# Kernel tuning notes

Measured on AMD Instinct MI355X. Metric: run time of the kernel, lower is better.

The kernel has to match this reference:

```python
import jax, jax.numpy as jnp
import numpy as np

M, K = 16384, 1024
E, N = 8, 5632  # N = 2 * intermediate (gate+up packed); intermediate = 2816
TOPK = 2


def setup_inputs() -> dict:
    key = jax.random.key(0)
    ks = jax.random.split(key, 5)
    return {
        "hidden_states": jax.random.normal(ks[0], (M, K), jnp.float32) * 0.05,
        "w1": jax.random.normal(ks[1], (E, N, K), jnp.float32) * 0.02,
        "w2": jax.random.normal(ks[2], (E, K, N // 2), jnp.float32) * 0.02,
        "topk_weights": jax.random.uniform(ks[3], (M, TOPK), jnp.float32),
        "topk_ids": jax.random.randint(ks[4], (M, TOPK), 0, E, jnp.int32),
    }


def reference(hidden_states, w1, w2, topk_weights, topk_ids):
    # hidden_states: [M, K]; w1: [E, N, K]; w2: [E, K, N//2]
    # topk_weights / topk_ids: [M, TOPK]
    m, k = hidden_states.shape
    e_num, n, _ = w1.shape
    topk = topk_ids.shape[1]
    half = n // 2
    out = jnp.zeros((m, topk, k), dtype=hidden_states.dtype)
    # Loop over the small fixed set of experts; each iteration is a dense GEMM
    # masked by the routing assignment (faithful to the grouped-GEMM math).
    for e in range(e_num):
        h1 = jnp.einsum('mk,nk->mn', hidden_states, w1[e])          # [M, N]
        gate, up = h1[:, :half], h1[:, half:]
        h2 = jax.nn.silu(gate) * up                                  # silu_and_mul
        o = jnp.einsum('mh,kh->mk', h2, w2[e])                       # [M, K]
        mask = (topk_ids == e).astype(o.dtype)                       # [M, TOPK]
        out = out + mask[:, :, None] * o[:, None, :]
    # multiply routed weights and sum over top-k slots
    return jnp.einsum('mtk,mt->mk', out, topk_weights)
```

## Files before the change

kernel.cpp:

```cpp
#include <hip/hip_runtime.h>
#include <hip/hip_bf16.h>

#define M_TOK 16384
#define K_DIM 1024
#define E_NUM 8
#define N_DIM 5632
#define HALF_N 2816
#define TOPK 2
#define NPAIR (M_TOK * TOPK)
#define BM 128
#define BK 64
#define BH1 128
#define BN2 256
#define NDESC (NPAIR / BM + E_NUM)
#define NHB1 (HALF_N / BH1)
#define NNB2 (K_DIM / BN2)

typedef short s16x4 __attribute__((ext_vector_type(4)));
typedef short s16x8 __attribute__((ext_vector_type(8)));
typedef float f32x4 __attribute__((ext_vector_type(4)));

__device__ __forceinline__ short f2bf(float f) {
  union { __hip_bfloat16 h; short s; } c;
  c.h = __float2bfloat16(f);
  return c.s;
}

__device__ __forceinline__ float bf2f(unsigned short s) {
  union { float f; unsigned u; } c;
  c.u = ((unsigned)s) << 16;
  return c.f;
}

__device__ __forceinline__ void gload_lds16(const void* g, void* l) {
  __builtin_amdgcn_global_load_lds(
      (const __attribute__((address_space(1))) unsigned int*)g,
      (__attribute__((address_space(3))) unsigned int*)l, 16, 0, 0);
}

__device__ __forceinline__ int xcd_work(int bid, int nwg) {
  const int xcd = bid & 7, loc = bid >> 3;
  const int q = nwg >> 3, r = nwg & 7;
  return (xcd < r ? xcd * (q + 1) : r * (q + 1) + (xcd - r) * q) + loc;
}

__global__ void cvt_f32_bf16_k(const float4* __restrict__ src,
                               s16x4* __restrict__ dst, int n4) {
  int i = blockIdx.x * blockDim.x + threadIdx.x;
  int stride = gridDim.x * blockDim.x;
  for (; i < n4; i += stride) {
    float4 f = src[i];
    s16x4 o = { f2bf(f.x), f2bf(f.y), f2bf(f.z), f2bf(f.w) };
    dst[i] = o;
  }
}

__global__ void moe_count(const int* __restrict__ ids, int* __restrict__ cnt) {
  const int p = blockIdx.x * 256 + threadIdx.x;
  const int e = ids[p];
  const int lane = threadIdx.x & 63;
  __shared__ int h[E_NUM];
  if (threadIdx.x < E_NUM) h[threadIdx.x] = 0;
  __syncthreads();
#pragma unroll
  for (int ex = 0; ex < E_NUM; ++ex) {
    unsigned long long m = __ballot(e == ex);
    if (lane == 0 && m) atomicAdd(&h[ex], __popcll(m));
  }
  __syncthreads();
  if (threadIdx.x < E_NUM) atomicAdd(&cnt[threadIdx.x], h[threadIdx.x]);
}

__global__ void moe_build(const int* __restrict__ cnt, int* __restrict__ offs,
                          int4* __restrict__ desc) {
  if (blockIdx.x == 0 && threadIdx.x == 0) {
    int o = 0, d = 0;
    for (int e = 0; e < E_NUM; ++e) {
      offs[e] = o;
      int end = o + cnt[e];
      for (int s = o; s < end; s += BM) desc[d++] = make_int4(e, s, end, 0);
      o = end;
    }
    offs[E_NUM] = o;
    while (d < NDESC) desc[d++] = make_int4(-1, 0, 0, 0);
  }
}

__global__ void moe_scatter(const int* __restrict__ ids, const float* __restrict__ tw,
                            const int* __restrict__ offs, int* __restrict__ fill,
                            int* __restrict__ tok, float* __restrict__ wgt,
                            int* __restrict__ inv) {
  const int p = blockIdx.x * 256 + threadIdx.x;
  const int e = ids[p];
  const int lane = threadIdx.x & 63;
  const int w = threadIdx.x >> 6;
  __shared__ int wcnt[4][E_NUM];
  __shared__ int wpre[4][E_NUM];
  __shared__ int base[E_NUM];
  const unsigned long long lt = (1ull << lane) - 1ull;
  int myrank = 0;
#pragma unroll
  for (int ex = 0; ex < E_NUM; ++ex) {
    unsigned long long m = __ballot(e == ex);
    if (e == ex) myrank = (int)__popcll(m & lt);
    if (lane == 0) wcnt[w][ex] = (int)__popcll(m);
  }
  __syncthreads();
  if (threadIdx.x < E_NUM) {
    const int ex = threadIdx.x;
    int s = 0;
#pragma unroll
    for (int ww = 0; ww < 4; ++ww) { wpre[ww][ex] = s; s += wcnt[ww][ex]; }
    base[ex] = atomicAdd(&fill[ex], s);
  }
  __syncthreads();
  const int pos = offs[e] + base[e] + wpre[w][e] + myrank;
  tok[pos] = p >> 1;
  wgt[pos] = tw[p];
  inv[p] = pos;
}

__global__ void moe_gather(const float* __restrict__ hs, const int* __restrict__ tok,
                           unsigned short* __restrict__ hsb) {
  const int pos = blockIdx.x;
  const int m = tok[pos];
  const int t = threadIdx.x;
  const float4* s = (const float4*)(hs + (size_t)m * K_DIM) + t * 2;
  const float4 a = s[0], b = s[1];
  s16x8 o = { f2bf(a.x), f2bf(a.y), f2bf(a.z), f2bf(a.w),
              f2bf(b.x), f2bf(b.y), f2bf(b.z), f2bf(b.w) };
  *(s16x8*)(hsb + (size_t)pos * K_DIM + t * 8) = o;
}

__launch_bounds__(512)
__global__ void moe_gemm1(const unsigned short* __restrict__ hsb,
                          const unsigned short* __restrict__ w1b,
                          const int4* __restrict__ desc,
                          unsigned short* __restrict__ h2) {
  const int work = xcd_work(blockIdx.x, NHB1 * NDESC);
  const int di = work / NHB1;
  const int hb = work - di * NHB1;
  const int4 d = desc[di];
  const int e = d.x;
  if (e < 0) return;
  const int pos0 = d.y, eend = d.z;
  const int h0 = hb * BH1;

  __shared__ __align__(16) unsigned short As[BM * BK];
  __shared__ __align__(16) unsigned short Gs[BH1 * BK];
  __shared__ __align__(16) unsigned short Us[BH1 * BK];

  const int tid = threadIdx.x;
  const int lane = tid & 63;
  const int wid = tid >> 6;
  const int wr = wid >> 2;
  const int wc = wid & 3;

  const unsigned short* Ab = hsb + (size_t)pos0 * K_DIM;
  const unsigned short* Gb = w1b + ((size_t)e * N_DIM + h0) * K_DIM;
  const unsigned short* Ub = Gb + (size_t)HALF_N * K_DIM;

  f32x4 accg[4][2], accu[4][2];
  const f32x4 z = {0.f, 0.f, 0.f, 0.f};
#pragma unroll
  for (int i = 0; i < 4; ++i)
#pragma unroll
    for (int j = 0; j < 2; ++j) { accg[i][j] = z; accu[i][j] = z; }

  const int lrow = lane >> 3;
  const int scol = ((lane & 7) ^ lrow) << 3;
  const int fr = lane & 15;
  const int fq = lane >> 4;
  const int sw = fr & 7;

  for (int kt = 0; kt < K_DIM / BK; ++kt) {
    const int k0 = kt * BK;
#pragma unroll
    for (int c = 0; c < 2; ++c) {
      const int seg = c * 8 + wid;
      const int row = seg * 8 + lrow;
      gload_lds16(Ab + (size_t)row * K_DIM + k0 + scol, &As[seg * 512]);
      gload_lds16(Gb + (size_t)row * K_DIM + k0 + scol, &Gs[seg * 512]);
      gload_lds16(Ub + (size_t)row * K_DIM + k0 + scol, &Us[seg * 512]);
    }
    __syncthreads();
#pragma unroll
    for (int s = 0; s < 2; ++s) {
      const int coff = (((s * 4 + fq) ^ sw) << 3);
      s16x8 af[4];
#pragma unroll
      for (int i = 0; i < 4; ++i)
        af[i] = *(const s16x8*)&As[(64 * wr + 16 * i + fr) * BK + coff];
      s16x8 gf[2], uf[2];
#pragma unroll
      for (int j = 0; j < 2; ++j) {
        const int hr = (32 * wc + 16 * j + fr) * BK + coff;
        gf[j] = *(const s16x8*)&Gs[hr];
        uf[j] = *(const s16x8*)&Us[hr];
      }
#pragma unroll
      for (int i = 0; i < 4; ++i)
#pragma unroll
        for (int j = 0; j < 2; ++j) {
          accg[i][j] = __builtin_amdgcn_mfma_f32_16x16x32_bf16(af[i], gf[j], accg[i][j], 0, 0, 0);
          accu[i][j] = __builtin_amdgcn_mfma_f32_16x16x32_bf16(af[i], uf[j], accu[i][j], 0, 0, 0);
        }
    }
    __syncthreads();
  }

  const int vlim = eend - pos0;
#pragma unroll
  for (int i = 0; i < 4; ++i) {
#pragma unroll
    for (int rr = 0; rr < 4; ++rr) {
      const int row = 64 * wr + 16 * i + fq * 4 + rr;
      if (row < vlim) {
        unsigned short* dst = h2 + (size_t)(pos0 + row) * HALF_N + h0 + 32 * wc;
#pragma unroll
        for (int j = 0; j < 2; ++j) {
          const float g = accg[i][j][rr];
          const float u = accu[i][j][rr];
          const float sg = g / (1.0f + __expf(-g));
          dst[16 * j + fr] = (unsigned short)f2bf(sg * u);
        }
      }
    }
  }
}

__launch_bounds__(512)
__global__ void moe_gemm2(const unsigned short* __restrict__ h2,
                          const unsigned short* __restrict__ w2b,
                          const int4* __restrict__ desc,
                          const float* __restrict__ wgt,
                          unsigned short* __restrict__ opair) {
  const int work = xcd_work(blockIdx.x, NNB2 * NDESC);
  const int di = work >> 2;
  const int nb = work & 3;
  const int4 d = desc[di];
  const int e = d.x;
  if (e < 0) return;
  const int pos0 = d.y, eend = d.z;
  const int n0 = nb * BN2;

  __shared__ __align__(16) unsigned short As[BM * BK];
  __shared__ __align__(16) unsigned short Bs[BN2 * BK];

  const int tid = threadIdx.x;
  const int lane = tid & 63;
  const int wid = tid >> 6;
  const int wr = wid >> 2;
  const int wc = wid & 3;

  const unsigned short* Ab = h2 + (size_t)pos0 * HALF_N;
  const unsigned short* Bb = w2b + ((size_t)e * K_DIM + n0) * HALF_N;

  f32x4 acc[4][4];
  const f32x4 z = {0.f, 0.f, 0.f, 0.f};
#pragma unroll
  for (int i = 0; i < 4; ++i)
#pragma unroll
    for (int j = 0; j < 4; ++j) acc[i][j] = z;

  const int lrow = lane >> 3;
  const int scol = ((lane & 7) ^ lrow) << 3;
  const int fr = lane & 15;
  const int fq = lane >> 4;
  const int sw = fr & 7;

  for (int ht = 0; ht < HALF_N / BK; ++ht) {
    const int k0 = ht * BK;
#pragma unroll
    for (int c = 0; c < 2; ++c) {
      const int seg = c * 8 + wid;
      const int row = seg * 8 + lrow;
      gload_lds16(Ab + (size_t)row * HALF_N + k0 + scol, &As[seg * 512]);
    }
#pragma unroll
    for (int c = 0; c < 4; ++c) {
      const int seg = c * 8 + wid;
      const int row = seg * 8 + lrow;
      gload_lds16(Bb + (size_t)row * HALF_N + k0 + scol, &Bs[seg * 512]);
    }
    __syncthreads();
#pragma unroll
    for (int s = 0; s < 2; ++s) {
      const int coff = (((s * 4 + fq) ^ sw) << 3);
      s16x8 af[4], bf[4];
#pragma unroll
      for (int i = 0; i < 4; ++i)
        af[i] = *(const s16x8*)&As[(64 * wr + 16 * i + fr) * BK + coff];
#pragma unroll
      for (int j = 0; j < 4; ++j)
        bf[j] = *(const s16x8*)&Bs[(64 * wc + 16 * j + fr) * BK + coff];
#pragma unroll
      for (int i = 0; i < 4; ++i)
#pragma unroll
        for (int j = 0; j < 4; ++j)
          acc[i][j] = __builtin_amdgcn_mfma_f32_16x16x32_bf16(af[i], bf[j], acc[i][j], 0, 0, 0);
    }
    __syncthreads();
  }

  const int vlim = eend - pos0;
#pragma unroll
  for (int i = 0; i < 4; ++i) {
#pragma unroll
    for (int rr = 0; rr < 4; ++rr) {
      const int row = 64 * wr + 16 * i + fq * 4 + rr;
      if (row < vlim) {
        const int pos = pos0 + row;
        const float wt = wgt[pos];
        unsigned short* dst = opair + (size_t)pos * K_DIM + n0 + 64 * wc;
#pragma unroll
        for (int j = 0; j < 4; ++j)
          dst[16 * j + fr] = (unsigned short)f2bf(wt * acc[i][j][rr]);
      }
    }
  }
}

__global__ void moe_combine(const unsigned short* __restrict__ opair,
                            const int* __restrict__ inv,
                            float* __restrict__ out) {
  const int m = blockIdx.x;
  const int t = threadIdx.x;
  const int p0 = inv[2 * m], p1 = inv[2 * m + 1];
  const s16x8 a = *(const s16x8*)&opair[(size_t)p0 * K_DIM + t * 8];
  const s16x8 b = *(const s16x8*)&opair[(size_t)p1 * K_DIM + t * 8];
  float4 o0, o1;
  o0.x = bf2f((unsigned short)a[0]) + bf2f((unsigned short)b[0]);
  o0.y = bf2f((unsigned short)a[1]) + bf2f((unsigned short)b[1]);
  o0.z = bf2f((unsigned short)a[2]) + bf2f((unsigned short)b[2]);
  o0.w = bf2f((unsigned short)a[3]) + bf2f((unsigned short)b[3]);
  o1.x = bf2f((unsigned short)a[4]) + bf2f((unsigned short)b[4]);
  o1.y = bf2f((unsigned short)a[5]) + bf2f((unsigned short)b[5]);
  o1.z = bf2f((unsigned short)a[6]) + bf2f((unsigned short)b[6]);
  o1.w = bf2f((unsigned short)a[7]) + bf2f((unsigned short)b[7]);
  float4* dst = (float4*)(out + (size_t)m * K_DIM + t * 8);
  dst[0] = o0;
  dst[1] = o1;
}

__global__ void sentinel_k(float* o) { o[0] = 1.0e9f; }

extern "C" void kernel_launch(void* const* d_in, const int* in_sizes, int n_in,
                              void* d_out, int out_size, void* d_ws, size_t ws_size,
                              hipStream_t stream) {
  const float* hs = (const float*)d_in[0];
  const float* w1 = (const float*)d_in[1];
  const float* w2 = (const float*)d_in[2];
  const float* tw = (const float*)d_in[3];
  const int* ids = (const int*)d_in[4];
  float* out = (float*)d_out;

  char* p = (char*)d_ws;
  auto carve = [&](size_t bytes) {
    char* r = p;
    p += (bytes + 255) & ~(size_t)255;
    return r;
  };
  unsigned short* w1b = (unsigned short*)carve((size_t)E_NUM * N_DIM * K_DIM * 2);
  unsigned short* w2b = (unsigned short*)carve((size_t)E_NUM * K_DIM * HALF_N * 2);
  unsigned short* hsb = (unsigned short*)carve((size_t)(NPAIR + BM) * K_DIM * 2);
  unsigned short* h2  = (unsigned short*)carve((size_t)(NPAIR + BM) * HALF_N * 2);
  int*   tok  = (int*)carve(NPAIR * 4);
  float* wgt  = (float*)carve(NPAIR * 4);
  int*   inv  = (int*)carve(NPAIR * 4);
  int*   meta = (int*)carve(1024);
  int4*  desc = (int4*)carve(NDESC * sizeof(int4));
  size_t need = (size_t)(p - (char*)d_ws);

  unsigned short* opair = hsb;

  if (need > ws_size) {
    hipMemsetAsync(d_out, 0, (size_t)out_size * sizeof(float), stream);
    sentinel_k<<<1, 1, 0, stream>>>(out);
    return;
  }

  int* cnt  = meta;
  int* fill = meta + 64;
  int* offs = meta + 128;

  hipMemsetAsync(meta, 0, 1024, stream);

  cvt_f32_bf16_k<<<2048, 256, 0, stream>>>(
      (const float4*)w1, (s16x4*)w1b, (int)((size_t)E_NUM * N_DIM * K_DIM / 4));
  cvt_f32_bf16_k<<<2048, 256, 0, stream>>>(
      (const float4*)w2, (s16x4*)w2b, (int)((size_t)E_NUM * K_DIM * HALF_N / 4));
  moe_count<<<NPAIR / 256, 256, 0, stream>>>(ids, cnt);
  moe_build<<<1, 64, 0, stream>>>(cnt, offs, desc);
  moe_scatter<<<NPAIR / 256, 256, 0, stream>>>(ids, tw, offs, fill, tok, wgt, inv);
  moe_gather<<<NPAIR, 128, 0, stream>>>(hs, tok, hsb);
  moe_gemm1<<<NHB1 * NDESC, 512, 0, stream>>>(hsb, w1b, desc, h2);
  moe_gemm2<<<NNB2 * NDESC, 512, 0, stream>>>(h2, w2b, desc, wgt, opair);
  moe_combine<<<M_TOK, 128, 0, stream>>>(opair, inv, out);
}
```

Before: 817.4 us.

## Switch MoE GEMMs to 32x32x16 MFMA with k-chunk-major LDS layout

Both grouped GEMM kernels now use the 32x32x16 bf16 MFMA instead of 16x16x32. The LDS tiles are re-laid out chunk-major: each 16-byte k-chunk for all rows is stored contiguously, which replaces the XOR swizzle and makes fragment reads linear. The aim is fewer MFMA issues and fewer LDS fragment loads per unit of work. The trade-offs are a different epilogue row mapping and non-contiguous per-thread global loads (each thread now reads one row at strided k offsets), which may hurt coalescing.

Measured after the change: 1.368 ms. 67.3% more time.

```diff
diff --git a/kernel.cpp b/kernel.cpp
--- a/kernel.cpp
+++ b/kernel.cpp
@@ -19,6 +19,7 @@
 typedef short s16x4 __attribute__((ext_vector_type(4)));
 typedef short s16x8 __attribute__((ext_vector_type(8)));
 typedef float f32x4 __attribute__((ext_vector_type(4)));
+typedef float f32x16 __attribute__((ext_vector_type(16)));
 
 __device__ __forceinline__ short f2bf(float f) {
   union { __hip_bfloat16 h; short s; } c;
@@ -155,75 +156,60 @@
   const int wid = tid >> 6;
   const int wr = wid >> 2;
   const int wc = wid & 3;
-
-  const unsigned short* Ab = hsb + (size_t)pos0 * K_DIM;
-  const unsigned short* Gb = w1b + ((size_t)e * N_DIM + h0) * K_DIM;
-  const unsigned short* Ub = Gb + (size_t)HALF_N * K_DIM;
-
-  f32x4 accg[4][2], accu[4][2];
-  const f32x4 z = {0.f, 0.f, 0.f, 0.f};
-#pragma unroll
-  for (int i = 0; i < 4; ++i)
-#pragma unroll
-    for (int j = 0; j < 2; ++j) { accg[i][j] = z; accu[i][j] = z; }
-
-  const int lrow = lane >> 3;
-  const int scol = ((lane & 7) ^ lrow) << 3;
-  const int fr = lane & 15;
-  const int fq = lane >> 4;
-  const int sw = fr & 7;
+  const int la = lane & 31;
+  const int hi = lane >> 5;
+
+  const int srow = tid & 127;
+  const int chA = tid >> 7;
+  const unsigned short* Ap = hsb + (size_t)(pos0 + srow) * K_DIM + chA * 8;
+  const unsigned short* Gp = w1b + ((size_t)e * N_DIM + h0 + srow) * K_DIM + chA * 8;
+  const unsigned short* Up = Gp + (size_t)HALF_N * K_DIM;
+
+  f32x16 accg[2], accu[2];
+#pragma unroll
+  for (int i = 0; i < 2; ++i) {
+#pragma unroll
+    for (int r = 0; r < 16; ++r) { accg[i][r] = 0.f; accu[i][r] = 0.f; }
+  }
 
   for (int kt = 0; kt < K_DIM / BK; ++kt) {
     const int k0 = kt * BK;
 #pragma unroll
     for (int c = 0; c < 2; ++c) {
-      const int seg = c * 8 + wid;
-      const int row = seg * 8 + lrow;
-      gload_lds16(Ab + (size_t)row * K_DIM + k0 + scol, &As[seg * 512]);
-      gload_lds16(Gb + (size_t)row * K_DIM + k0 + scol, &Gs[seg * 512]);
-      gload_lds16(Ub + (size_t)row * K_DIM + k0 + scol, &Us[seg * 512]);
+      const int goff = (c * 512 + tid) * 8;
+      const int koff = k0 + c * 32;
+      gload_lds16(Ap + koff, &As[goff]);
+      gload_lds16(Gp + koff, &Gs[goff]);
+      gload_lds16(Up + koff, &Us[goff]);
     }
     __syncthreads();
 #pragma unroll
-    for (int s = 0; s < 2; ++s) {
-      const int coff = (((s * 4 + fq) ^ sw) << 3);
-      s16x8 af[4];
-#pragma unroll
-      for (int i = 0; i < 4; ++i)
-        af[i] = *(const s16x8*)&As[(64 * wr + 16 * i + fr) * BK + coff];
-      s16x8 gf[2], uf[2];
-#pragma unroll
-      for (int j = 0; j < 2; ++j) {
-        const int hr = (32 * wc + 16 * j + fr) * BK + coff;
-        gf[j] = *(const s16x8*)&Gs[hr];
-        uf[j] = *(const s16x8*)&Us[hr];
-      }
-#pragma unroll
-      for (int i = 0; i < 4; ++i)
-#pragma unroll
-        for (int j = 0; j < 2; ++j) {
-          accg[i][j] = __builtin_amdgcn_mfma_f32_16x16x32_bf16(af[i], gf[j], accg[i][j], 0, 0, 0);
-          accu[i][j] = __builtin_amdgcn_mfma_f32_16x16x32_bf16(af[i], uf[j], accu[i][j], 0, 0, 0);
-        }
+    for (int ks = 0; ks < 4; ++ks) {
+      const int cb = ((ks * 2 + hi) << 7);
+      s16x8 af0 = *(const s16x8*)&As[(cb + 64 * wr + la) * 8];
+      s16x8 af1 = *(const s16x8*)&As[(cb + 64 * wr + 32 + la) * 8];
+      s16x8 gf  = *(const s16x8*)&Gs[(cb + 32 * wc + la) * 8];
+      s16x8 uf  = *(const s16x8*)&Us[(cb + 32 * wc + la) * 8];
+      accg[0] = __builtin_amdgcn_mfma_f32_32x32x16_bf16(af0, gf, accg[0], 0, 0, 0);
+      accu[0] = __builtin_amdgcn_mfma_f32_32x32x16_bf16(af0, uf, accu[0], 0, 0, 0);
+      accg[1] = __builtin_amdgcn_mfma_f32_32x32x16_bf16(af1, gf, accg[1], 0, 0, 0);
+      accu[1] = __builtin_amdgcn_mfma_f32_32x32x16_bf16(af1, uf, accu[1], 0, 0, 0);
     }
     __syncthreads();
   }
 
   const int vlim = eend - pos0;
 #pragma unroll
-  for (int i = 0; i < 4; ++i) {
-#pragma unroll
-    for (int rr = 0; rr < 4; ++rr) {
-      const int row = 64 * wr + 16 * i + fq * 4 + rr;
+  for (int i = 0; i < 2; ++i) {
+#pragma unroll
+    for (int r = 0; r < 16; ++r) {
+      const int row = 64 * wr + 32 * i + (r & 3) + 8 * (r >> 2) + 4 * hi;
       if (row < vlim) {
-        unsigned short* dst = h2 + (size_t)(pos0 + row) * HALF_N + h0 + 32 * wc;
-#pragma unroll
-        for (int j = 0; j < 2; ++j) {
-          const float g = accg[i][j][rr];
-          const float u = accu[i][j][rr];
-          const float sg = g / (1.0f + __expf(-g));
-          dst[16 * j + fr] = (unsigned short)f2bf(sg * u);
-        }
+        const float g = accg[i][r];
+        const float u = accu[i][r];
+        const float sg = g / (1.0f + __expf(-g));
+        h2[(size_t)(pos0 + row) * HALF_N + h0 + 32 * wc + la] =
+            (unsigned short)f2bf(sg * u);
       }
     }
   }
@@ -252,70 +238,63 @@
   const int wid = tid >> 6;
   const int wr = wid >> 2;
   const int wc = wid & 3;
-
-  const unsigned short* Ab = h2 + (size_t)pos0 * HALF_N;
-  const unsigned short* Bb = w2b + ((size_t)e * K_DIM + n0) * HALF_N;
-
-  f32x4 acc[4][4];
-  const f32x4 z = {0.f, 0.f, 0.f, 0.f};
-#pragma unroll
-  for (int i = 0; i < 4; ++i)
-#pragma unroll
-    for (int j = 0; j < 4; ++j) acc[i][j] = z;
-
-  const int lrow = lane >> 3;
-  const int scol = ((lane & 7) ^ lrow) << 3;
-  const int fr = lane & 15;
-  const int fq = lane >> 4;
-  const int sw = fr & 7;
+  const int la = lane & 31;
+  const int hi = lane >> 5;
+
+  const int sarow = tid & 127;
+  const int chA = tid >> 7;
+  const unsigned short* Ap = h2 + (size_t)(pos0 + sarow) * HALF_N + chA * 8;
+  const int sbrow = tid & 255;
+  const int chB = tid >> 8;
+  const unsigned short* Bp = w2b + ((size_t)e * K_DIM + n0 + sbrow) * HALF_N + chB * 8;
+
+  f32x16 acc[2][2];
+#pragma unroll
+  for (int i = 0; i < 2; ++i)
+#pragma unroll
+    for (int j = 0; j < 2; ++j)
+#pragma unroll
+      for (int r = 0; r < 16; ++r) acc[i][j][r] = 0.f;
 
   for (int ht = 0; ht < HALF_N / BK; ++ht) {
     const int k0 = ht * BK;
 #pragma unroll
     for (int c = 0; c < 2; ++c) {
-      const int seg = c * 8 + wid;
-      const int row = seg * 8 + lrow;
-      gload_lds16(Ab + (size_t)row * HALF_N + k0 + scol, &As[seg * 512]);
+      gload_lds16(Ap + k0 + c * 32, &As[(c * 512 + tid) * 8]);
     }
 #pragma unroll
     for (int c = 0; c < 4; ++c) {
-      const int seg = c * 8 + wid;
-      const int row = seg * 8 + lrow;
-      gload_lds16(Bb + (size_t)row * HALF_N + k0 + scol, &Bs[seg * 512]);
+      gload_lds16(Bp + k0 + c * 16, &Bs[(c * 512 + tid) * 8]);
     }
     __syncthreads();
 #pragma unroll
-    for (int s = 0; s < 2; ++s) {
-      const int coff = (((s * 4 + fq) ^ sw) << 3);
-      s16x8 af[4], bf[4];
-#pragma unroll
-      for (int i = 0; i < 4; ++i)
-        af[i] = *(const s16x8*)&As[(64 * wr + 16 * i + fr) * BK + coff];
-#pragma unroll
-      for (int j = 0; j < 4; ++j)
-        bf[j] = *(const s16x8*)&Bs[(64 * wc + 16 * j + fr) * BK + coff];
-#pragma unroll
-      for (int i = 0; i < 4; ++i)
-#pragma unroll
-        for (int j = 0; j < 4; ++j)
-          acc[i][j] = __builtin_amdgcn_mfma_f32_16x16x32_bf16(af[i], bf[j], acc[i][j], 0, 0, 0);
+    for (int ks = 0; ks < 4; ++ks) {
+      const int cbA = ((ks * 2 + hi) << 7);
+      const int cbB = ((ks * 2 + hi) << 8);
+      s16x8 af0 = *(const s16x8*)&As[(cbA + 64 * wr + la) * 8];
+      s16x8 af1 = *(const s16x8*)&As[(cbA + 64 * wr + 32 + la) * 8];
+      s16x8 bf0 = *(const s16x8*)&Bs[(cbB + 64 * wc + la) * 8];
+      s16x8 bf1 = *(const s16x8*)&Bs[(cbB + 64 * wc + 32 + la) * 8];
+      acc[0][0] = __builtin_amdgcn_mfma_f32_32x32x16_bf16(af0, bf0, acc[0][0], 0, 0, 0);
+      acc[0][1] = __builtin_amdgcn_mfma_f32_32x32x16_bf16(af0, bf1, acc[0][1], 0, 0, 0);
+      acc[1][0] = __builtin_amdgcn_mfma_f32_32x32x16_bf16(af1, bf0, acc[1][0], 0, 0, 0);
+      acc[1][1] = __builtin_amdgcn_mfma_f32_32x32x16_bf16(af1, bf1, acc[1][1], 0, 0, 0);
     }
     __syncthreads();
   }
 
   const int vlim = eend - pos0;
 #pragma unroll
-  for (int i = 0; i < 4; ++i) {
-#pragma unroll
-    for (int rr = 0; rr < 4; ++rr) {
-      const int row = 64 * wr + 16 * i + fq * 4 + rr;
+  for (int i = 0; i < 2; ++i) {
+#pragma unroll
+    for (int r = 0; r < 16; ++r) {
+      const int row = 64 * wr + 32 * i + (r & 3) + 8 * (r >> 2) + 4 * hi;
       if (row < vlim) {
         const int pos = pos0 + row;
         const float wt = wgt[pos];
         unsigned short* dst = opair + (size_t)pos * K_DIM + n0 + 64 * wc;
-#pragma unroll
-        for (int j = 0; j < 4; ++j)
-          dst[16 * j + fr] = (unsigned short)f2bf(wt * acc[i][j][rr]);
+        dst[la]      = (unsigned short)f2bf(wt * acc[i][0][r]);
+        dst[32 + la] = (unsigned short)f2bf(wt * acc[i][1][r]);
       }
     }
   }
```
